# Kernel optimization log

Hardware: AMD Instinct MI355X
Metric: run time of the kernel (lower is better)

## Reference

```python
import jax, jax.numpy as jnp
import numpy as np

B, T, TAU = 4, 512, 512
D_MODEL = 1024  # in_dim == out_dim (required: pos embedding dim out_dim feeds pos_proj with in_size=in_dim)
H, D = 16, 64
LN_EPS = 1e-5


def rel_shift(x):
    # x: [B, T, L, H] -> Transformer-XL relative shift
    b, t, l, h = x.shape
    x = jnp.pad(x, ((0, 0), (0, 0), (1, 0), (0, 0)))  # pad j-dim front
    x = x.reshape(b, l + 1, t, h)[:, 1:, :, :]
    return x.reshape(b, t, l, h)


def setup_inputs() -> dict:
    key = jax.random.key(0)
    ks = jax.random.split(key, 7)
    s = 0.02
    return {
        "inputs": jax.random.normal(ks[0], (B, T, D_MODEL), jnp.float32),
        "memory": jax.random.normal(ks[1], (B, TAU, D_MODEL), jnp.float32),
        "w_qkv": jax.random.normal(ks[2], (3 * H * D, D_MODEL), jnp.float32) * s,
        "w_pos": jax.random.normal(ks[3], (H * D, D_MODEL), jnp.float32) * s,
        "w_out": jax.random.normal(ks[4], (D_MODEL, H * D), jnp.float32) * s,
        "uvar": jax.random.normal(ks[5], (H, D), jnp.float32) * s,
        "vvar": jax.random.normal(ks[6], (H, D), jnp.float32) * s,
        "ln_gamma": jnp.ones((D_MODEL,), jnp.float32),
        "ln_beta": jnp.zeros((D_MODEL,), jnp.float32),
    }


def reference(inputs, memory, w_qkv, w_pos, w_out, uvar, vvar, ln_gamma, ln_beta):
    b, t, din = inputs.shape
    tau = memory.shape[1]
    L = tau + t
    h, d = uvar.shape

    x = jnp.concatenate([jax.lax.stop_gradient(memory), inputs], axis=1)  # [B,L,Din]
    # input layernorm
    mu = jnp.mean(x, axis=-1, keepdims=True)
    var = jnp.mean((x - mu) ** 2, axis=-1, keepdims=True)
    x = (x - mu) / jnp.sqrt(var + LN_EPS) * ln_gamma + ln_beta

    qkv = x @ w_qkv.T  # [B,L,3HD]
    q, k, v = jnp.split(qkv, 3, axis=-1)
    q = q[:, -t:].reshape(b, t, h, d)
    k = k.reshape(b, L, h, d)
    v = v.reshape(b, L, h, d)

    # sinusoidal relative position embedding, dim = out_dim (= din here)
    inv_freq = 1.0 / (10000.0 ** (jnp.arange(0, din, 2, dtype=jnp.float32) / din))
    pos = jnp.arange(L - 1, -1, -1, dtype=jnp.float32)
    sin_in = pos[:, None] * inv_freq[None, :]                 # [L, din/2]
    phi = jnp.concatenate([jnp.sin(sin_in), jnp.cos(sin_in)], axis=-1)  # [L, din]
    R = (phi @ w_pos.T).reshape(L, h, d)

    score = jnp.einsum('bihd,bjhd->bijh', q + uvar, k)        # content score
    pos_score = jnp.einsum('bihd,jhd->bijh', q + vvar, R)     # position score
    score = (score + rel_shift(pos_score)) / (d ** 0.5)       # [B,T,L,H]

    # causal mask: query i attends to j <= tau + i
    mask = (jnp.arange(L)[None, :] <= (tau + jnp.arange(t))[:, None]).astype(score.dtype)
    mask = mask[None, :, :, None]
    masked = score * mask + 1e30 * (mask - 1.0)
    w = jax.nn.softmax(masked, axis=2)

    out = jnp.einsum('bijh,bjhd->bihd', w, v).reshape(b, t, h * d)
    return out @ w_out.T
```

## Files before the change

### kernel.cpp

```cpp
#include <hip/hip_runtime.h>
#include <math.h>

#define B_   4
#define T_   512
#define TAU_ 512
#define L_   1024
#define DM_  1024
#define H_   16
#define D_   64

typedef short  s16x8 __attribute__((ext_vector_type(8)));
typedef ushort u16x4 __attribute__((ext_vector_type(4)));
typedef float  f32x4 __attribute__((ext_vector_type(4)));

__device__ __forceinline__ ushort f2bf(float x) {
  uint u = __float_as_uint(x);
  u += 0x7fffu + ((u >> 16) & 1u);
  return (ushort)(u >> 16);
}
__device__ __forceinline__ float bf2f(ushort u) {
  return __uint_as_float(((uint)u) << 16);
}
__device__ __forceinline__ int sw64(int row, int col) {
  return row * 64 + (col ^ ((row & 7) << 3));
}

__global__ __launch_bounds__(256) void prep_kernel(
    const float* __restrict__ inp, const float* __restrict__ mem,
    const float* __restrict__ gamma, const float* __restrict__ beta,
    ushort* __restrict__ xn, ushort* __restrict__ phi,
    const float* __restrict__ wq, ushort* __restrict__ wqb,
    const float* __restrict__ wp, ushort* __restrict__ wpb,
    const float* __restrict__ wo, ushort* __restrict__ wob) {
  int blk = blockIdx.x;
  int t = threadIdx.x;
  if (blk < 4096) {
    int row = blk;
    int b = row >> 10, l = row & 1023;
    const float* src = (l < TAU_)
        ? mem + ((size_t)b * TAU_ + l) * DM_
        : inp + ((size_t)b * T_ + (l - TAU_)) * DM_;
    float4 v = *(const float4*)(src + t * 4);
    float s  = v.x + v.y + v.z + v.w;
    float s2 = v.x * v.x + v.y * v.y + v.z * v.z + v.w * v.w;
#pragma unroll
    for (int off = 32; off > 0; off >>= 1) {
      s  += __shfl_down(s, off);
      s2 += __shfl_down(s2, off);
    }
    __shared__ float red[8];
    __shared__ float stat[2];
    int wid = t >> 6;
    if ((t & 63) == 0) { red[wid * 2] = s; red[wid * 2 + 1] = s2; }
    __syncthreads();
    if (t == 0) {
      float ts  = red[0] + red[2] + red[4] + red[6];
      float ts2 = red[1] + red[3] + red[5] + red[7];
      float mu  = ts * (1.0f / DM_);
      float var = ts2 * (1.0f / DM_) - mu * mu;
      stat[0] = mu;
      stat[1] = 1.0f / sqrtf(var + 1e-5f);
    }
    __syncthreads();
    float mu = stat[0], rstd = stat[1];
    float4 g  = *(const float4*)(gamma + t * 4);
    float4 be = *(const float4*)(beta  + t * 4);
    u16x4 o;
    o[0] = f2bf((v.x - mu) * rstd * g.x + be.x);
    o[1] = f2bf((v.y - mu) * rstd * g.y + be.y);
    o[2] = f2bf((v.z - mu) * rstd * g.z + be.z);
    o[3] = f2bf((v.w - mu) * rstd * g.w + be.w);
    *(u16x4*)(xn + (size_t)row * DM_ + t * 4) = o;
  } else if (blk < 8192) {
    int idx = (blk - 4096) * 256 + t;
    int m = idx >> 10, c = idx & 1023;
    float p = (float)(1023 - m);
    int cc = (c < 512) ? c : c - 512;
    float invf = __expf(-((float)(2 * cc) * (1.0f / 1024.0f)) * 9.210340371976184f);
    float a = p * invf;
    phi[idx] = f2bf((c < 512) ? sinf(a) : cosf(a));
  } else {
    int i = (blk - 8192) * 256 + t;
    const float* src; ushort* dst; int off;
    if (i < 786432)       { src = wq; dst = wqb; off = i; }
    else if (i < 1048576) { src = wp; dst = wpb; off = i - 786432; }
    else                  { src = wo; dst = wob; off = i - 1048576; }
    float4 v = *(const float4*)(src + (size_t)off * 4);
    u16x4 o = { f2bf(v.x), f2bf(v.y), f2bf(v.z), f2bf(v.w) };
    *(u16x4*)(dst + (size_t)off * 4) = o;
  }
}

template <typename CT>
__device__ __forceinline__ void gemm_nt_body(
    const ushort* __restrict__ A, const ushort* __restrict__ B,
    CT* __restrict__ C, int M, int N, int K, int bx, int by) {
  __shared__ __attribute__((aligned(16))) ushort As[128 * 64];
  __shared__ __attribute__((aligned(16))) ushort Bs[128 * 64];
  int t = threadIdx.x;
  int w = t >> 6, lane = t & 63, g = lane >> 4, low = lane & 15;
  int wr = w >> 1, wc = w & 1;
  int m0 = by * 128, n0 = bx * 128;
  f32x4 acc[4][4] = {};

  for (int kt = 0; kt < K; kt += 64) {
    __syncthreads();
#pragma unroll
    for (int q = 0; q < 4; ++q) {
      int c = t + q * 256;
      int row = c >> 3;
      int gslot = (c & 7) ^ (row & 7);
      const ushort* ga = A + (size_t)(m0 + row) * K + kt + gslot * 8;
      const ushort* gb = B + (size_t)(n0 + row) * K + kt + gslot * 8;
      __builtin_amdgcn_global_load_lds(
          (const __attribute__((address_space(1))) void*)ga,
          (__attribute__((address_space(3))) void*)&As[(q * 256 + w * 64) * 8],
          16, 0, 0);
      __builtin_amdgcn_global_load_lds(
          (const __attribute__((address_space(1))) void*)gb,
          (__attribute__((address_space(3))) void*)&Bs[(q * 256 + w * 64) * 8],
          16, 0, 0);
    }
    __syncthreads();

#pragma unroll
    for (int kc = 0; kc < 2; ++kc) {
      s16x8 af[4], bfr[4];
#pragma unroll
      for (int mi = 0; mi < 4; ++mi) {
        int row = wr * 64 + mi * 16 + low;
        af[mi] = *(const s16x8*)&As[row * 64 + (((4 * kc + g) ^ (row & 7)) * 8)];
      }
#pragma unroll
      for (int ni = 0; ni < 4; ++ni) {
        int col = wc * 64 + ni * 16 + low;
        bfr[ni] = *(const s16x8*)&Bs[col * 64 + (((4 * kc + g) ^ (col & 7)) * 8)];
      }
#pragma unroll
      for (int mi = 0; mi < 4; ++mi)
#pragma unroll
        for (int ni = 0; ni < 4; ++ni)
          acc[mi][ni] = __builtin_amdgcn_mfma_f32_16x16x32_bf16(
              af[mi], bfr[ni], acc[mi][ni], 0, 0, 0);
    }
  }
#pragma unroll
  for (int mi = 0; mi < 4; ++mi)
#pragma unroll
    for (int ni = 0; ni < 4; ++ni)
#pragma unroll
      for (int r = 0; r < 4; ++r) {
        int m = m0 + wr * 64 + mi * 16 + 4 * g + r;
        int n = n0 + wc * 64 + ni * 16 + low;
        if constexpr (sizeof(CT) == 2)
          C[(size_t)m * N + n] = f2bf(acc[mi][ni][r]);
        else
          C[(size_t)m * N + n] = acc[mi][ni][r];
      }
}

__global__ __launch_bounds__(256) void qkv_r_gemm(
    const ushort* __restrict__ xnb, const ushort* __restrict__ wqb,
    ushort* __restrict__ qkvB,
    const ushort* __restrict__ phib, const ushort* __restrict__ wpb,
    ushort* __restrict__ RmB) {
  int orig = blockIdx.x;
  int id = (orig & 7) * 104 + (orig >> 3);
  if (id < 768)
    gemm_nt_body<ushort>(xnb, wqb, qkvB, 4096, 3072, 1024, id % 24, id / 24);
  else {
    id -= 768;
    gemm_nt_body<ushort>(phib, wpb, RmB, 1024, 1024, 1024, id % 8, id / 8);
  }
}

__global__ __launch_bounds__(256) void out_gemm(
    const ushort* __restrict__ attnb, const ushort* __restrict__ wob,
    float* __restrict__ out) {
  int orig = blockIdx.x;
  int id = (orig & 7) * 16 + (orig >> 3);
  gemm_nt_body<float>(attnb, wob, out, 2048, 1024, 1024, id % 8, id / 8);
}

__global__ __launch_bounds__(256) void vtrans_kernel(
    const ushort* __restrict__ qkv, ushort* __restrict__ vtg) {
  __shared__ ushort vs[64 * 65];
  int bid = blockIdx.x;
  int lt = bid & 15;
  int h  = (bid >> 4) & 15;
  int b  = bid >> 8;
  int l0 = lt * 64;
  int t = threadIdx.x;
#pragma unroll
  for (int q = 0; q < 2; ++q) {
    int c = t + q * 256;
    int row = c >> 3, sl = c & 7;
    s16x8 v = *(const s16x8*)(qkv +
        (size_t)(b * L_ + l0 + row) * 3072 + 2048 + h * 64 + sl * 8);
#pragma unroll
    for (int e = 0; e < 8; ++e) vs[row * 65 + sl * 8 + e] = (ushort)v[e];
  }
  __syncthreads();
#pragma unroll
  for (int q = 0; q < 2; ++q) {
    int c = t + q * 256;
    int d = c >> 3, sl = c & 7;
    s16x8 o;
#pragma unroll
    for (int e = 0; e < 8; ++e) o[e] = (short)vs[(sl * 8 + e) * 65 + d];
    *(s16x8*)(vtg + (size_t)((b * 16 + h) * 64 + d) * 1024 + l0 + sl * 8) = o;
  }
}

__global__ __launch_bounds__(256) void attn_mfma_kernel(
    const ushort* __restrict__ qkv, const ushort* __restrict__ Rm,
    const ushort* __restrict__ vtg,
    const float* __restrict__ uvar, const float* __restrict__ vvar,
    ushort* __restrict__ attn) {
  __shared__ __attribute__((aligned(16))) ushort Ks[2][64 * 64];
  __shared__ __attribute__((aligned(16))) ushort Vt[2][64 * 64];
  __shared__ __attribute__((aligned(16))) ushort Rs[2][128 * 64];
  __shared__ __attribute__((aligned(16))) ushort Pp[4][16 * 64];

  int t   = threadIdx.x;
  int w   = t >> 6;
  int lw  = t & 63;
  int g   = lw >> 4;
  int low = lw & 15;

  int bid = blockIdx.x;
  int bi  = bid & 7;
  int h   = (bid >> 3) & 15;
  int b   = bid >> 7;
  int i0  = bi * 64;
  int lb_w = 48 - 16 * w;

  auto stage = [&](int buf, int tl) {
    int j0s = tl * 64;
#pragma unroll
    for (int q = 0; q < 2; ++q) {
      int c = t + q * 256;
      int row = c >> 3;
      int sl = (c & 7) ^ (row & 7);
      const ushort* srck = qkv + (size_t)(b * L_ + j0s + row) * 3072 +
                           1024 + h * 64 + sl * 8;
      __builtin_amdgcn_global_load_lds(
          (const __attribute__((address_space(1))) void*)srck,
          (__attribute__((address_space(3))) void*)&Ks[buf][(q * 256 + w * 64) * 8],
          16, 0, 0);
      const ushort* srcv = vtg + (size_t)((b * 16 + h) * 64 + row) * 1024 +
                           j0s + sl * 8;
      __builtin_amdgcn_global_load_lds(
          (const __attribute__((address_space(1))) void*)srcv,
          (__attribute__((address_space(3))) void*)&Vt[buf][(q * 256 + w * 64) * 8],
          16, 0, 0);
    }
    int mb = j0s + 448 - i0;
#pragma unroll
    for (int q = 0; q < 4; ++q) {
      int c = t + q * 256;
      int row = c >> 3;
      int m = mb + row; m = (m > 1023) ? 1023 : m;
      int sl = (c & 7) ^ (row & 7);
      const ushort* srcr = Rm + (size_t)m * 1024 + h * 64 + sl * 8;
      __builtin_amdgcn_global_load_lds(
          (const __attribute__((address_space(1))) void*)srcr,
          (__attribute__((address_space(3))) void*)&Rs[buf][(q * 256 + w * 64) * 8],
          16, 0, 0);
    }
  };

  int iq = i0 + 16 * w + low;
  s16x8 qu[2], qv[2];
  {
    const ushort* qrow = qkv + (size_t)(b * L_ + TAU_ + iq) * 3072 + h * 64;
    const float* ur = uvar + h * 64;
    const float* vr = vvar + h * 64;
#pragma unroll
    for (int kc = 0; kc < 2; ++kc) {
      int dbase = kc * 32 + 8 * g;
#pragma unroll
      for (int e = 0; e < 8; ++e) {
        float q = bf2f(qrow[dbase + e]);
        qu[kc][e] = (short)f2bf(q + ur[dbase + e]);
        qv[kc][e] = (short)f2bf(q + vr[dbase + e]);
      }
    }
  }

  f32x4 O[4] = {};
  float mreg[4] = {-INFINITY, -INFINITY, -INFINITY, -INFINITY};
  float lreg[4] = {0.f, 0.f, 0.f, 0.f};

  int ntiles = 9 + bi;
  stage(0, 0);
  __syncthreads();
  int cur = 0;
  for (int tile = 0; tile < ntiles; ++tile) {
    int j0 = tile * 64;
    if (tile + 1 < ntiles) stage(cur ^ 1, tile + 1);

    f32x4 s[4] = {};
#pragma unroll
    for (int jt = 0; jt < 4; ++jt) {
#pragma unroll
      for (int kc = 0; kc < 2; ++kc) {
        s16x8 kb = *(const s16x8*)&Ks[cur][sw64(jt * 16 + low, kc * 32 + 8 * g)];
        s[jt] = __builtin_amdgcn_mfma_f32_16x16x32_bf16(qu[kc], kb, s[jt], 0, 0, 0);
      }
    }
    f32x4 p[5] = {};
#pragma unroll
    for (int mt = 0; mt < 5; ++mt) {
#pragma unroll
      for (int kc = 0; kc < 2; ++kc) {
        s16x8 rb = *(const s16x8*)&Rs[cur][sw64(lb_w + mt * 16 + low, kc * 32 + 8 * g)];
        p[mt] = __builtin_amdgcn_mfma_f32_16x16x32_bf16(qv[kc], rb, p[mt], 0, 0, 0);
      }
    }
#pragma unroll
    for (int r = 0; r < 4; ++r) {
      int iL = 4 * g + r;
      int src = g * 16 + ((low + 15 - iL) & 15);
      float sh0 = __shfl(p[0][r], src);
      float sh1 = __shfl(p[1][r], src);
      float sh2 = __shfl(p[2][r], src);
      float sh3 = __shfl(p[3][r], src);
      float sh4 = __shfl(p[4][r], src);
      bool lo = (low <= iL);
      float po0 = lo ? sh0 : sh1;
      float po1 = lo ? sh1 : sh2;
      float po2 = lo ? sh2 : sh3;
      float po3 = lo ? sh3 : sh4;
      int lim = TAU_ + i0 + 16 * w + iL;
      s[0][r] = (j0 +  0 + low <= lim) ? (s[0][r] + po0) * 0.125f : -1e30f;
      s[1][r] = (j0 + 16 + low <= lim) ? (s[1][r] + po1) * 0.125f : -1e30f;
      s[2][r] = (j0 + 32 + low <= lim) ? (s[2][r] + po2) * 0.125f : -1e30f;
      s[3][r] = (j0 + 48 + low <= lim) ? (s[3][r] + po3) * 0.125f : -1e30f;
    }
#pragma unroll
    for (int r = 0; r < 4; ++r) {
      float mx = fmaxf(fmaxf(s[0][r], s[1][r]), fmaxf(s[2][r], s[3][r]));
      mx = fmaxf(mx, __shfl_xor(mx, 1));
      mx = fmaxf(mx, __shfl_xor(mx, 2));
      mx = fmaxf(mx, __shfl_xor(mx, 4));
      mx = fmaxf(mx, __shfl_xor(mx, 8));
      float mn = fmaxf(mreg[r], mx);
      float alpha = __expf(mreg[r] - mn);
      mreg[r] = mn;
      float sum = 0.f;
#pragma unroll
      for (int jt = 0; jt < 4; ++jt) {
        float pe = __expf(s[jt][r] - mn);
        s[jt][r] = pe;
        sum += pe;
      }
      sum += __shfl_xor(sum, 1);
      sum += __shfl_xor(sum, 2);
      sum += __shfl_xor(sum, 4);
      sum += __shfl_xor(sum, 8);
      lreg[r] = lreg[r] * alpha + sum;
      O[0][r] *= alpha; O[1][r] *= alpha; O[2][r] *= alpha; O[3][r] *= alpha;
    }
#pragma unroll
    for (int jt = 0; jt < 4; ++jt)
#pragma unroll
      for (int r = 0; r < 4; ++r)
        Pp[w][sw64(4 * g + r, jt * 16 + low)] = f2bf(s[jt][r]);
    asm volatile("s_waitcnt lgkmcnt(0)" ::: "memory");
    s16x8 pa0 = *(const s16x8*)&Pp[w][sw64(low, 8 * g)];
    s16x8 pa1 = *(const s16x8*)&Pp[w][sw64(low, 32 + 8 * g)];
#pragma unroll
    for (int dt = 0; dt < 4; ++dt) {
      s16x8 v0 = *(const s16x8*)&Vt[cur][sw64(dt * 16 + low, 8 * g)];
      s16x8 v1 = *(const s16x8*)&Vt[cur][sw64(dt * 16 + low, 32 + 8 * g)];
      O[dt] = __builtin_amdgcn_mfma_f32_16x16x32_bf16(pa0, v0, O[dt], 0, 0, 0);
      O[dt] = __builtin_amdgcn_mfma_f32_16x16x32_bf16(pa1, v1, O[dt], 0, 0, 0);
    }
    __syncthreads();
    cur ^= 1;
  }
  float inv[4];
#pragma unroll
  for (int r = 0; r < 4; ++r) inv[r] = 1.0f / lreg[r];
#pragma unroll
  for (int dt = 0; dt < 4; ++dt)
#pragma unroll
    for (int r = 0; r < 4; ++r)
      attn[((size_t)(b * T_ + i0 + 16 * w + 4 * g + r)) * 1024 +
           h * 64 + dt * 16 + low] = f2bf(O[dt][r] * inv[r]);
}

extern "C" void kernel_launch(void* const* d_in, const int* in_sizes, int n_in,
                              void* d_out, int out_size, void* d_ws, size_t ws_size,
                              hipStream_t stream) {
  const float* inputs = (const float*)d_in[0];
  const float* memory = (const float*)d_in[1];
  const float* w_qkv  = (const float*)d_in[2];
  const float* w_pos  = (const float*)d_in[3];
  const float* w_out  = (const float*)d_in[4];
  const float* uvar   = (const float*)d_in[5];
  const float* vvar   = (const float*)d_in[6];
  const float* gamma  = (const float*)d_in[7];
  const float* beta   = (const float*)d_in[8];
  float* out = (float*)d_out;

  ushort* qkvB = (ushort*)d_ws;
  ushort* xnb  = qkvB + (size_t)4096 * 3072;
  ushort* phib = xnb  + (size_t)4096 * 1024;
  ushort* RmB  = phib + (size_t)1024 * 1024;
  ushort* wqb  = RmB  + (size_t)1024 * 1024;
  ushort* wpb  = wqb  + (size_t)3072 * 1024;
  ushort* wob  = wpb  + (size_t)1024 * 1024;
  ushort* vtg  = wob  + (size_t)1024 * 1024;
  ushort* attnb = xnb;

  prep_kernel<<<13312, 256, 0, stream>>>(inputs, memory, gamma, beta, xnb,
                                         phib, w_qkv, wqb, w_pos, wpb, w_out, wob);
  qkv_r_gemm<<<832, 256, 0, stream>>>(xnb, wqb, qkvB, phib, wpb, RmB);
  vtrans_kernel<<<B_ * H_ * 16, 256, 0, stream>>>(qkvB, vtg);
  attn_mfma_kernel<<<dim3(B_ * H_ * 8), 256, 0, stream>>>(qkvB, RmB, vtg, uvar, vvar, attnb);
  out_gemm<<<128, 256, 0, stream>>>(attnb, wob, out);
}
```

Measured before the change: 212.1 us.

## Fuse V transpose into attention kernel and use DPP for row reductions

Drops the separate V-transpose kernel. The attention kernel now loads V rows from the qkv buffer into registers one tile ahead and writes them transposed and swizzled into LDS after the PV MFMAs. This removes one kernel launch and a global round trip of transposed V. The cost is scalar LDS stores in every tile and extra register pressure. Separately, the xor shuffles in the softmax max and sum reductions are replaced with DPP row moves, which avoid LDS-routed shuffle traffic.

```diff
diff --git a/kernel.cpp b/kernel.cpp
--- a/kernel.cpp
+++ b/kernel.cpp
@@ -23,6 +23,12 @@
 }
 __device__ __forceinline__ int sw64(int row, int col) {
   return row * 64 + (col ^ ((row & 7) << 3));
+}
+template <int CTRL>
+__device__ __forceinline__ float dppmov(float x) {
+  int xi = __float_as_int(x);
+  return __int_as_float(
+      __builtin_amdgcn_update_dpp(xi, xi, CTRL, 0xF, 0xF, false));
 }
 
 __global__ __launch_bounds__(256) void prep_kernel(
@@ -182,39 +188,8 @@
   gemm_nt_body<float>(attnb, wob, out, 2048, 1024, 1024, id % 8, id / 8);
 }
 
-__global__ __launch_bounds__(256) void vtrans_kernel(
-    const ushort* __restrict__ qkv, ushort* __restrict__ vtg) {
-  __shared__ ushort vs[64 * 65];
-  int bid = blockIdx.x;
-  int lt = bid & 15;
-  int h  = (bid >> 4) & 15;
-  int b  = bid >> 8;
-  int l0 = lt * 64;
-  int t = threadIdx.x;
-#pragma unroll
-  for (int q = 0; q < 2; ++q) {
-    int c = t + q * 256;
-    int row = c >> 3, sl = c & 7;
-    s16x8 v = *(const s16x8*)(qkv +
-        (size_t)(b * L_ + l0 + row) * 3072 + 2048 + h * 64 + sl * 8);
-#pragma unroll
-    for (int e = 0; e < 8; ++e) vs[row * 65 + sl * 8 + e] = (ushort)v[e];
-  }
-  __syncthreads();
-#pragma unroll
-  for (int q = 0; q < 2; ++q) {
-    int c = t + q * 256;
-    int d = c >> 3, sl = c & 7;
-    s16x8 o;
-#pragma unroll
-    for (int e = 0; e < 8; ++e) o[e] = (short)vs[(sl * 8 + e) * 65 + d];
-    *(s16x8*)(vtg + (size_t)((b * 16 + h) * 64 + d) * 1024 + l0 + sl * 8) = o;
-  }
-}
-
 __global__ __launch_bounds__(256) void attn_mfma_kernel(
     const ushort* __restrict__ qkv, const ushort* __restrict__ Rm,
-    const ushort* __restrict__ vtg,
     const float* __restrict__ uvar, const float* __restrict__ vvar,
     ushort* __restrict__ attn) {
   __shared__ __attribute__((aligned(16))) ushort Ks[2][64 * 64];
@@ -235,7 +210,7 @@
   int i0  = bi * 64;
   int lb_w = 48 - 16 * w;
 
-  auto stage = [&](int buf, int tl) {
+  auto stage_kr = [&](int buf, int tl) {
     int j0s = tl * 64;
 #pragma unroll
     for (int q = 0; q < 2; ++q) {
@@ -248,12 +223,6 @@
           (const __attribute__((address_space(1))) void*)srck,
           (__attribute__((address_space(3))) void*)&Ks[buf][(q * 256 + w * 64) * 8],
           16, 0, 0);
-      const ushort* srcv = vtg + (size_t)((b * 16 + h) * 64 + row) * 1024 +
-                           j0s + sl * 8;
-      __builtin_amdgcn_global_load_lds(
-          (const __attribute__((address_space(1))) void*)srcv,
-          (__attribute__((address_space(3))) void*)&Vt[buf][(q * 256 + w * 64) * 8],
-          16, 0, 0);
     }
     int mb = j0s + 448 - i0;
 #pragma unroll
@@ -270,6 +239,27 @@
     }
   };
 
+  int vj  = t & 63;
+  int vd0 = (t >> 6) * 8;
+  float4 vreg[2];
+  auto vload = [&](int tl) {
+    const ushort* p = qkv + (size_t)(b * L_ + tl * 64 + vj) * 3072 + 2048 + h * 64;
+    vreg[0] = *(const float4*)(p + vd0);
+    vreg[1] = *(const float4*)(p + vd0 + 32);
+  };
+  auto vwrite = [&](int buf) {
+#pragma unroll
+    for (int it = 0; it < 2; ++it) {
+      ushort vals[8];
+      *(float4*)vals = vreg[it];
+#pragma unroll
+      for (int e = 0; e < 8; ++e) {
+        int d = it * 32 + vd0 + e;
+        Vt[buf][d * 64 + (vj ^ ((d & 7) << 3))] = vals[e];
+      }
+    }
+  };
+
   int iq = i0 + 16 * w + low;
   s16x8 qu[2], qv[2];
   {
@@ -293,12 +283,15 @@
   float lreg[4] = {0.f, 0.f, 0.f, 0.f};
 
   int ntiles = 9 + bi;
-  stage(0, 0);
+  stage_kr(0, 0);
+  vload(0);
+  vwrite(0);
   __syncthreads();
   int cur = 0;
   for (int tile = 0; tile < ntiles; ++tile) {
     int j0 = tile * 64;
-    if (tile + 1 < ntiles) stage(cur ^ 1, tile + 1);
+    bool more = (tile + 1 < ntiles);
+    if (more) { stage_kr(cur ^ 1, tile + 1); vload(tile + 1); }
 
     f32x4 s[4] = {};
 #pragma unroll
@@ -341,10 +334,10 @@
 #pragma unroll
     for (int r = 0; r < 4; ++r) {
       float mx = fmaxf(fmaxf(s[0][r], s[1][r]), fmaxf(s[2][r], s[3][r]));
-      mx = fmaxf(mx, __shfl_xor(mx, 1));
-      mx = fmaxf(mx, __shfl_xor(mx, 2));
-      mx = fmaxf(mx, __shfl_xor(mx, 4));
-      mx = fmaxf(mx, __shfl_xor(mx, 8));
+      mx = fmaxf(mx, dppmov<0xB1>(mx));
+      mx = fmaxf(mx, dppmov<0x4E>(mx));
+      mx = fmaxf(mx, dppmov<0x124>(mx));
+      mx = fmaxf(mx, dppmov<0x128>(mx));
       float mn = fmaxf(mreg[r], mx);
       float alpha = __expf(mreg[r] - mn);
       mreg[r] = mn;
@@ -355,10 +348,10 @@
         s[jt][r] = pe;
         sum += pe;
       }
-      sum += __shfl_xor(sum, 1);
-      sum += __shfl_xor(sum, 2);
-      sum += __shfl_xor(sum, 4);
-      sum += __shfl_xor(sum, 8);
+      sum += dppmov<0xB1>(sum);
+      sum += dppmov<0x4E>(sum);
+      sum += dppmov<0x124>(sum);
+      sum += dppmov<0x128>(sum);
       lreg[r] = lreg[r] * alpha + sum;
       O[0][r] *= alpha; O[1][r] *= alpha; O[2][r] *= alpha; O[3][r] *= alpha;
     }
@@ -377,6 +370,7 @@
       O[dt] = __builtin_amdgcn_mfma_f32_16x16x32_bf16(pa0, v0, O[dt], 0, 0, 0);
       O[dt] = __builtin_amdgcn_mfma_f32_16x16x32_bf16(pa1, v1, O[dt], 0, 0, 0);
     }
+    if (more) vwrite(cur ^ 1);
     __syncthreads();
     cur ^= 1;
   }
@@ -412,13 +406,11 @@
   ushort* wqb  = RmB  + (size_t)1024 * 1024;
   ushort* wpb  = wqb  + (size_t)3072 * 1024;
   ushort* wob  = wpb  + (size_t)1024 * 1024;
-  ushort* vtg  = wob  + (size_t)1024 * 1024;
   ushort* attnb = xnb;
 
   prep_kernel<<<13312, 256, 0, stream>>>(inputs, memory, gamma, beta, xnb,
                                          phib, w_qkv, wqb, w_pos, wpb, w_out, wob);
   qkv_r_gemm<<<832, 256, 0, stream>>>(xnb, wqb, qkvB, phib, wpb, RmB);
-  vtrans_kernel<<<B_ * H_ * 16, 256, 0, stream>>>(qkvB, vtg);
-  attn_mfma_kernel<<<dim3(B_ * H_ * 8), 256, 0, stream>>>(qkvB, RmB, vtg, uvar, vvar, attnb);
+  attn_mfma_kernel<<<dim3(B_ * H_ * 8), 256, 0, stream>>>(qkvB, RmB, uvar, vvar, attnb);
   out_gemm<<<128, 256, 0, stream>>>(attnb, wob, out);
 }
```

Result: no change. 211.2 us (-0.4%).
